# Optimization experiments

Hardware: AMD Instinct MI355X
Metric: run time of the kernel (lower is better)

## Reference

```python
import jax, jax.numpy as jnp
import numpy as np

N_NODES = 50000
N_EDGES = 800000
HEADS = 4
IN_CH = 64
# hidden_dims=[32,64] reversed -> per-head out channels [64, 32]; concat=True
C1, C2 = 64, 32          # layer per-head channels
OUT_CH = 64              # conv_recon per-head channels, concat=False
NEG_SLOPE = 0.2


def gat_conv(x, edge_src, edge_dst, W, a_src, a_dst, b, concat):
    """PyG GATConv (v1) forward, eval mode (no dropout).
    x: [N, F_in]; W: [F_in, H*C]; a_src/a_dst: [H, C]; b: [H*C] or [C].
    edge (j -> i): messages flow edge_src -> edge_dst; softmax grouped by dst.
    """
    N = x.shape[0]
    H, C = a_src.shape
    h = (x @ W).reshape(N, H, C)                    # [N, H, C]
    al_s = jnp.einsum('nhc,hc->nh', h, a_src)       # [N, H]
    al_d = jnp.einsum('nhc,hc->nh', h, a_dst)       # [N, H]
    e = al_s[edge_src] + al_d[edge_dst]             # [E, H]
    e = jax.nn.leaky_relu(e, negative_slope=NEG_SLOPE)
    # segment softmax over incoming edges of each dst node
    m = jax.ops.segment_max(e, edge_dst, num_segments=N)          # [N, H]
    ex = jnp.exp(e - m[edge_dst])                                  # [E, H]
    s = jax.ops.segment_sum(ex, edge_dst, num_segments=N)         # [N, H]
    alpha = ex / (s[edge_dst] + 1e-16)                             # [E, H]
    msg = h[edge_src] * alpha[:, :, None]                          # [E, H, C]
    out = jax.ops.segment_sum(msg, edge_dst, num_segments=N)      # [N, H, C]
    out = out.reshape(N, H * C) if concat else out.mean(axis=1)
    return out + b


def setup_inputs() -> dict:
    key = jax.random.key(0)
    ks = jax.random.split(key, 16)
    sc = 0.1
    inp = {
        'x': jax.random.normal(ks[0], (N_NODES, IN_CH), jnp.float32),
        'edge_index': jax.random.randint(ks[1], (2, N_EDGES), 0, N_NODES, jnp.int64),
        # layer 1: in 64 -> 4 heads x 64, concat -> 256
        'W1': jax.random.normal(ks[2], (IN_CH, HEADS * C1), jnp.float32) * sc,
        'a1_src': jax.random.normal(ks[3], (HEADS, C1), jnp.float32) * sc,
        'a1_dst': jax.random.normal(ks[4], (HEADS, C1), jnp.float32) * sc,
        'b1': jnp.zeros((HEADS * C1,), jnp.float32),
        # layer 2: in 256 -> 4 heads x 32, concat -> 128
        'W2': jax.random.normal(ks[5], (HEADS * C1, HEADS * C2), jnp.float32) * sc,
        'a2_src': jax.random.normal(ks[6], (HEADS, C2), jnp.float32) * sc,
        'a2_dst': jax.random.normal(ks[7], (HEADS, C2), jnp.float32) * sc,
        'b2': jnp.zeros((HEADS * C2,), jnp.float32),
        # conv_recon: in 128 -> 4 heads x 64, concat=False (mean) -> 64
        'W3': jax.random.normal(ks[8], (HEADS * C2, HEADS * OUT_CH), jnp.float32) * sc,
        'a3_src': jax.random.normal(ks[9], (HEADS, OUT_CH), jnp.float32) * sc,
        'a3_dst': jax.random.normal(ks[10], (HEADS, OUT_CH), jnp.float32) * sc,
        'b3': jnp.zeros((OUT_CH,), jnp.float32),
    }
    return inp


def reference(x, edge_index, W1, a1_src, a1_dst, b1, W2, a2_src, a2_dst, b2,
              W3, a3_src, a3_dst, b3):
    src, dst = edge_index[0], edge_index[1]
    # used_DSBN=False -> no norm/ReLU between layers (matches torch forward)
    h = gat_conv(x, src, dst, W1, a1_src, a1_dst, b1, concat=True)
    h = gat_conv(h, src, dst, W2, a2_src, a2_dst, b2, concat=True)
    recon = gat_conv(h, src, dst, W3, a3_src, a3_dst, b3, concat=False)
    return recon
```

## Files before the change

### kernel.cpp

```cpp
#include <hip/hip_runtime.h>
#include <hip/hip_bf16.h>

#define HEADS 4

typedef __attribute__((ext_vector_type(4))) float f32x4;
typedef __attribute__((ext_vector_type(8))) short s16x8;

__device__ __forceinline__ float u2f(unsigned short u) {
    return __uint_as_float(((unsigned)u) << 16);
}
__device__ __forceinline__ unsigned short rne(float v) {
    unsigned b = __float_as_uint(v);
    return (unsigned short)((b + 0x7FFF + ((b >> 16) & 1)) >> 16);
}
__device__ __forceinline__ float ld1(const float* p) { return *p; }
__device__ __forceinline__ float ld1(const __hip_bfloat16* p) {
    return u2f(*reinterpret_cast<const unsigned short*>(p));
}
__device__ __forceinline__ float2 ld2(const float* p) { return *reinterpret_cast<const float2*>(p); }
__device__ __forceinline__ float2 ld2(const __hip_bfloat16* p) {
    ushort2 u = *reinterpret_cast<const ushort2*>(p);
    return make_float2(u2f(u.x), u2f(u.y));
}
__device__ __forceinline__ float4 ld4(const float* p) { return *reinterpret_cast<const float4*>(p); }
__device__ __forceinline__ float4 ld4(const __hip_bfloat16* p) {
    ushort4 u = *reinterpret_cast<const ushort4*>(p);
    return make_float4(u2f(u.x), u2f(u.y), u2f(u.z), u2f(u.w));
}
__device__ __forceinline__ void st1(float* p, float v) { *p = v; }
__device__ __forceinline__ void st1(__hip_bfloat16* p, float v) {
    *reinterpret_cast<unsigned short*>(p) = rne(v);
}
__device__ __forceinline__ void st2(float* p, float a, float b) {
    *reinterpret_cast<float2*>(p) = make_float2(a, b);
}
__device__ __forceinline__ void st2(__hip_bfloat16* p, float a, float b) {
    *reinterpret_cast<ushort2*>(p) = make_ushort2(rne(a), rne(b));
}
__device__ __forceinline__ void st4(float* p, float4 v) { *reinterpret_cast<float4*>(p) = v; }
__device__ __forceinline__ void st4(__hip_bfloat16* p, float4 v) {
    *reinterpret_cast<ushort4*>(p) = make_ushort4(rne(v.x), rne(v.y), rne(v.z), rne(v.w));
}

__device__ __forceinline__ int detect64(const int* __restrict__ e) {
    return ((e[1] | e[3] | e[5] | e[7]) == 0) ? 1 : 0;
}
__device__ __forceinline__ int edge_elem(const int* e, size_t idx, int is64) {
    return is64 ? e[2 * idx] : e[idx];
}

__global__ void deg_kernel(const int* __restrict__ eidx, int* __restrict__ deg, int E, int N) {
    int e = blockIdx.x * blockDim.x + threadIdx.x;
    if (e < E) {
        int is64 = detect64(eidx);
        int d = edge_elem(eidx, (size_t)E + e, is64);
        if ((unsigned)d < (unsigned)N) atomicAdd(&deg[d], 1);
    }
}

__global__ void reduce_kernel(const int* __restrict__ deg, int* __restrict__ bsum, int n) {
    __shared__ int sdata[256];
    int base = blockIdx.x * 1024;
    int t = threadIdx.x;
    int v = 0;
#pragma unroll
    for (int j = 0; j < 4; ++j) {
        int i = base + t + j * 256;
        if (i < n) v += deg[i];
    }
    sdata[t] = v;
    __syncthreads();
    for (int off = 128; off > 0; off >>= 1) {
        if (t < off) sdata[t] += sdata[t + off];
        __syncthreads();
    }
    if (t == 0) bsum[blockIdx.x] = sdata[0];
}

__global__ void scan_bsum_kernel(const int* __restrict__ bsum, int* __restrict__ boff,
                                 int nb, int* __restrict__ totalp) {
    int lane = threadIdx.x;
    int carry = 0;
    for (int base = 0; base < nb; base += 64) {
        int i = base + lane;
        int v = (i < nb) ? bsum[i] : 0;
        int inc = v;
        for (int off = 1; off < 64; off <<= 1) {
            int tt = __shfl_up(inc, off);
            if (lane >= off) inc += tt;
        }
        if (i < nb) boff[i] = carry + inc - v;
        carry += __shfl(inc, 63);
    }
    if (lane == 0) *totalp = carry;
}

__global__ void block_scan_kernel(const int* __restrict__ deg, const int* __restrict__ boff,
                                  int* __restrict__ rowptr, int* __restrict__ cursor, int n) {
    __shared__ int wsum[4];
    int base = blockIdx.x * 1024;
    int t = threadIdx.x;
    int lane = t & 63, w = t >> 6;
    int v[4];
    int lsum = 0;
#pragma unroll
    for (int j = 0; j < 4; ++j) {
        int i = base + t * 4 + j;
        v[j] = (i < n) ? deg[i] : 0;
        lsum += v[j];
    }
    int inc = lsum;
    for (int off = 1; off < 64; off <<= 1) {
        int tt = __shfl_up(inc, off);
        if (lane >= off) inc += tt;
    }
    if (lane == 63) wsum[w] = inc;
    __syncthreads();
    int woff = 0;
    for (int i = 0; i < w; ++i) woff += wsum[i];
    int ex = boff[blockIdx.x] + woff + inc - lsum;
#pragma unroll
    for (int j = 0; j < 4; ++j) {
        int i = base + t * 4 + j;
        if (i < n) { rowptr[i] = ex; cursor[i] = ex; }
        ex += v[j];
    }
}

__global__ void scatter_kernel(const int* __restrict__ eidx, int* __restrict__ cursor,
                               int* __restrict__ csr_src, int E, int N) {
    int e = blockIdx.x * blockDim.x + threadIdx.x;
    if (e < E) {
        int is64 = detect64(eidx);
        int s = edge_elem(eidx, (size_t)e, is64);
        int d = edge_elem(eidx, (size_t)E + e, is64);
        if ((unsigned)d < (unsigned)N && (unsigned)s < (unsigned)N) {
            int pos = atomicAdd(&cursor[d], 1);
            csr_src[pos] = s;
        }
    }
}

__global__ void prep_kernel(const float* __restrict__ x,
                            const float* __restrict__ W1, const float* __restrict__ W2,
                            const float* __restrict__ W3, const float* __restrict__ b1,
                            const float* __restrict__ a1s, const float* __restrict__ a1d,
                            const float* __restrict__ a3s, const float* __restrict__ a3d,
                            __hip_bfloat16* __restrict__ xb,
                            __hip_bfloat16* __restrict__ Bt3, __hip_bfloat16* __restrict__ BtF,
                            float* __restrict__ bias12,
                            float* __restrict__ ps1, float* __restrict__ pd1,
                            float* __restrict__ ps3, float* __restrict__ pd3, int n8) {
    int b = blockIdx.x, t = threadIdx.x;
    int nXB = (n8 + 255) / 256;
    if (b < nXB) {
        int i = b * 256 + t;
        if (i < n8) {
            float4 a = *reinterpret_cast<const float4*>(&x[(size_t)i * 8]);
            float4 c = *reinterpret_cast<const float4*>(&x[(size_t)i * 8 + 4]);
            st4(&xb[(size_t)i * 8], a);
            st4(&xb[(size_t)i * 8 + 4], c);
        }
        return;
    }
    b -= nXB;
    if (b < 128) {
        int idx = b * 256 + t;
        int c = idx >> 9, r = idx & 511;
        int h = r >> 7, kk = r & 127;
        st1(&Bt3[idx], W3[(size_t)kk * 256 + h * 64 + c] * 0.25f);
        return;
    }
    b -= 128;
    if (b < 128) {
        int idx = b * 256 + t;
        int m = idx >> 8, k = idx & 255;
        int h = k >> 6, kin = k & 63;
        float acc = 0.f;
        for (int c = 0; c < 64; ++c)
            acc += W1[(size_t)kin * 256 + h * 64 + c] * W2[(size_t)(h * 64 + c) * 128 + m];
        st1(&BtF[idx], acc);
        return;
    }
    b -= 128;
    if (b < 1) {
        if (t < 128) {
            float acc = 0.f;
            for (int j = 0; j < 256; ++j) acc += b1[j] * W2[(size_t)j * 128 + t];
            bias12[t] = acc;
        }
        return;
    }
    b -= 1;
    if (b < 1) {
        int h = t >> 6, k = t & 63;
        float ss = 0.f, sd = 0.f;
        for (int c = 0; c < 64; ++c) {
            float w = W1[(size_t)k * 256 + h * 64 + c];
            ss += w * a1s[h * 64 + c];
            sd += w * a1d[h * 64 + c];
        }
        ps1[t] = ss;
        pd1[t] = sd;
        return;
    }
    b -= 1;
    if (b < 2) {
        int idx = b * 256 + t;
        int h = idx >> 7, k = idx & 127;
        float ss = 0.f, sd = 0.f;
        for (int c = 0; c < 64; ++c) {
            float w = W3[(size_t)k * 256 + h * 64 + c];
            ss += w * a3s[h * 64 + c];
            sd += w * a3d[h * 64 + c];
        }
        ps3[idx] = ss;
        pd3[idx] = sd;
        return;
    }
}

template <int K, typename T>
__global__ void alx_kernel(const T* __restrict__ x, const float* __restrict__ ps,
                           const float* __restrict__ pd, float* __restrict__ als,
                           float* __restrict__ ald, int N) {
    int idx = blockIdx.x * blockDim.x + threadIdx.x;
    if (idx >= N * 4) return;
    int n = idx >> 2, h = idx & 3;
    const T* row = x + (size_t)n * K;
    const float* vs = ps + h * K;
    const float* vd = pd + h * K;
    float ss = 0.f, sd = 0.f;
#pragma unroll
    for (int c = 0; c < K; c += 4) {
        float4 v = ld4(&row[c]);
        float4 a = *reinterpret_cast<const float4*>(&vs[c]);
        float4 b = *reinterpret_cast<const float4*>(&vd[c]);
        ss += v.x * a.x + v.y * a.y + v.z * a.z + v.w * a.w;
        sd += v.x * b.x + v.y * b.y + v.z * b.z + v.w * b.w;
    }
    als[idx] = ss;
    ald[idx] = sd;
}

template <int C, typename T>
__global__ void al_kernel(const T* __restrict__ h,
                          const float* __restrict__ a_src, const float* __restrict__ a_dst,
                          float* __restrict__ al_s, float* __restrict__ al_d, int N) {
    int idx = blockIdx.x * blockDim.x + threadIdx.x;
    if (idx >= N * HEADS) return;
    int n = idx >> 2, hd = idx & 3;
    const T* row = h + (size_t)n * HEADS * C + hd * C;
    float ss = 0.f, sd = 0.f;
#pragma unroll
    for (int c = 0; c < C; c += 4) {
        float4 v = ld4(&row[c]);
        float4 as = *reinterpret_cast<const float4*>(&a_src[hd * C + c]);
        float4 ad = *reinterpret_cast<const float4*>(&a_dst[hd * C + c]);
        ss += v.x * as.x + v.y * as.y + v.z * as.z + v.w * as.w;
        sd += v.x * ad.x + v.y * ad.y + v.z * ad.z + v.w * ad.w;
    }
    al_s[idx] = ss;
    al_d[idx] = sd;
}

template <int K, typename TIN, typename TOUT>
__global__ void gather_pre_kernel(const TIN* __restrict__ x, const float* __restrict__ als,
                                  const float* __restrict__ ald, const int* __restrict__ rowptr,
                                  const int* __restrict__ csr, TOUT* __restrict__ agg, int N) {
    constexpr int V = K / 64;
    int wave = (blockIdx.x * blockDim.x + threadIdx.x) >> 6;
    int lane = threadIdx.x & 63;
    if (wave >= N) return;
    int h4 = lane & 3, e4 = lane >> 2;
    float aldv = ald[wave * 4 + h4];
    float s0 = 0.f, s1 = 0.f, s2 = 0.f, s3 = 0.f;
    float acc[4][V] = {};
    int beg = rowptr[wave], end = rowptr[wave + 1];
    for (int kc = beg; kc < end; kc += 16) {
        int cnt = end - kc;
        if (cnt > 16) cnt = 16;
        int j = kc + e4;
        int src = csr[(j < end) ? j : beg];
        float e = als[src * 4 + h4] + aldv;
        e = fmaxf(e, 0.2f * e);
        float myw = __expf(e);
        if (cnt == 16) {
            int sj[16];
#pragma unroll
            for (int jj = 0; jj < 16; ++jj) sj[jj] = __shfl(src, jj * 4);
            if (V == 1) {
                float pv[16];
#pragma unroll
                for (int jj = 0; jj < 16; ++jj) pv[jj] = ld1(&x[(size_t)sj[jj] * K + lane]);
#pragma unroll
                for (int jj = 0; jj < 16; ++jj) {
                    float w0 = __shfl(myw, jj * 4 + 0), w1 = __shfl(myw, jj * 4 + 1);
                    float w2 = __shfl(myw, jj * 4 + 2), w3 = __shfl(myw, jj * 4 + 3);
                    s0 += w0; s1 += w1; s2 += w2; s3 += w3;
                    acc[0][0] += w0 * pv[jj]; acc[1][0] += w1 * pv[jj];
                    acc[2][0] += w2 * pv[jj]; acc[3][0] += w3 * pv[jj];
                }
            } else {
                float2 pv[16];
#pragma unroll
                for (int jj = 0; jj < 16; ++jj) pv[jj] = ld2(&x[(size_t)sj[jj] * K + lane * 2]);
#pragma unroll
                for (int jj = 0; jj < 16; ++jj) {
                    float w0 = __shfl(myw, jj * 4 + 0), w1 = __shfl(myw, jj * 4 + 1);
                    float w2 = __shfl(myw, jj * 4 + 2), w3 = __shfl(myw, jj * 4 + 3);
                    s0 += w0; s1 += w1; s2 += w2; s3 += w3;
                    acc[0][0] += w0 * pv[jj].x; acc[0][1] += w0 * pv[jj].y;
                    acc[1][0] += w1 * pv[jj].x; acc[1][1] += w1 * pv[jj].y;
                    acc[2][0] += w2 * pv[jj].x; acc[2][1] += w2 * pv[jj].y;
                    acc[3][0] += w3 * pv[jj].x; acc[3][1] += w3 * pv[jj].y;
                }
            }
        } else {
            for (int jj = 0; jj < cnt; ++jj) {
                int sjj = __shfl(src, jj * 4);
                float w0 = __shfl(myw, jj * 4 + 0), w1 = __shfl(myw, jj * 4 + 1);
                float w2 = __shfl(myw, jj * 4 + 2), w3 = __shfl(myw, jj * 4 + 3);
                s0 += w0; s1 += w1; s2 += w2; s3 += w3;
                if (V == 1) {
                    float v = ld1(&x[(size_t)sjj * K + lane]);
                    acc[0][0] += w0 * v; acc[1][0] += w1 * v;
                    acc[2][0] += w2 * v; acc[3][0] += w3 * v;
                } else {
                    float2 v = ld2(&x[(size_t)sjj * K + lane * 2]);
                    acc[0][0] += w0 * v.x; acc[0][1] += w0 * v.y;
                    acc[1][0] += w1 * v.x; acc[1][1] += w1 * v.y;
                    acc[2][0] += w2 * v.x; acc[2][1] += w2 * v.y;
                    acc[3][0] += w3 * v.x; acc[3][1] += w3 * v.y;
                }
            }
        }
    }
    float inv[4] = {1.f / (s0 + 1e-16f), 1.f / (s1 + 1e-16f),
                    1.f / (s2 + 1e-16f), 1.f / (s3 + 1e-16f)};
    size_t o = (size_t)wave * 4 * K;
#pragma unroll
    for (int h = 0; h < 4; ++h) {
        if (V == 1) {
            st1(&agg[o + h * K + lane], acc[h][0] * inv[h]);
        } else {
            st2(&agg[o + h * K + lane * 2], acc[h][0] * inv[h], acc[h][1] * inv[h]);
        }
    }
}

template <typename TIN, typename TOUT>
__global__ void gather_post32_alx_kernel(const TIN* __restrict__ h2, const float* __restrict__ als,
                                         const float* __restrict__ ald, const int* __restrict__ rowptr,
                                         const int* __restrict__ csr, const float* __restrict__ bias,
                                         const float* __restrict__ ps3, const float* __restrict__ pd3,
                                         TOUT* __restrict__ outp,
                                         float* __restrict__ als3, float* __restrict__ ald3, int N) {
    int wave = (blockIdx.x * blockDim.x + threadIdx.x) >> 6;
    int lane = threadIdx.x & 63;
    if (wave >= N) return;
    int h4 = lane & 3, e4 = lane >> 2;
    int hh = lane >> 4, l16 = lane & 15;
    float aldv = ald[wave * 4 + h4];
    float s = 0.f, a0 = 0.f, a1 = 0.f;
    int beg = rowptr[wave], end = rowptr[wave + 1];
    for (int kc = beg; kc < end; kc += 16) {
        int cnt = end - kc;
        if (cnt > 16) cnt = 16;
        int j = kc + e4;
        int src = csr[(j < end) ? j : beg];
        float e = als[src * 4 + h4] + aldv;
        e = fmaxf(e, 0.2f * e);
        float myw = __expf(e);
        if (cnt == 16) {
            int sj[16];
#pragma unroll
            for (int jj = 0; jj < 16; ++jj) sj[jj] = __shfl(src, jj * 4);
            float2 pv[16];
#pragma unroll
            for (int jj = 0; jj < 16; ++jj)
                pv[jj] = ld2(&h2[(size_t)sj[jj] * 128 + hh * 32 + l16 * 2]);
#pragma unroll
            for (int jj = 0; jj < 16; ++jj) {
                float w = __shfl(myw, jj * 4 + hh);
                s += w;
                a0 += w * pv[jj].x;
                a1 += w * pv[jj].y;
            }
        } else {
            for (int jj = 0; jj < cnt; ++jj) {
                int sjj = __shfl(src, jj * 4);
                float w = __shfl(myw, jj * 4 + hh);
                s += w;
                float2 v = ld2(&h2[(size_t)sjj * 128 + hh * 32 + l16 * 2]);
                a0 += w * v.x;
                a1 += w * v.y;
            }
        }
    }
    float inv = 1.f / (s + 1e-16f);
    int c = hh * 32 + l16 * 2;
    float v0 = a0 * inv + bias[c];
    float v1 = a1 * inv + bias[c + 1];
    st2(&outp[(size_t)wave * 128 + c], v0, v1);

    float sArr[4], dArr[4];
#pragma unroll
    for (int h = 0; h < 4; ++h) {
        float2 vs = *reinterpret_cast<const float2*>(&ps3[h * 128 + c]);
        float2 vd = *reinterpret_cast<const float2*>(&pd3[h * 128 + c]);
        sArr[h] = v0 * vs.x + v1 * vs.y;
        dArr[h] = v0 * vd.x + v1 * vd.y;
    }
#pragma unroll
    for (int off = 1; off < 64; off <<= 1) {
#pragma unroll
        for (int h = 0; h < 4; ++h) {
            sArr[h] += __shfl_xor(sArr[h], off);
            dArr[h] += __shfl_xor(dArr[h], off);
        }
    }
    if (lane < 4) {
        float os = (lane == 0) ? sArr[0] : (lane == 1) ? sArr[1] : (lane == 2) ? sArr[2] : sArr[3];
        float od = (lane == 0) ? dArr[0] : (lane == 1) ? dArr[1] : (lane == 2) ? dArr[2] : dArr[3];
        als3[wave * 4 + lane] = os;
        ald3[wave * 4 + lane] = od;
    }
}

template <typename TOUT>
__global__ __launch_bounds__(256) void mfma_gemm_kernel(
    const __hip_bfloat16* __restrict__ A, int lda, int aSel,
    const __hip_bfloat16* __restrict__ Bt,
    TOUT* __restrict__ O, int ldo,
    const float* __restrict__ bias, int N, int K) {
    __shared__ __hip_bfloat16 As[128][40];
    __shared__ __hip_bfloat16 Bs[64][40];
    int col0 = blockIdx.x * 64;
    int row0 = blockIdx.y * 128;
    int aOff = aSel ? col0 : 0;
    int tid = threadIdx.x;
    int wv = tid >> 6, lane = tid & 63;
    int g = lane >> 4, l16 = lane & 15;
    f32x4 acc[2][4] = {};

    for (int k0 = 0; k0 < K; k0 += 32) {
#pragma unroll
        for (int i = 0; i < 2; ++i) {
            int idx = tid + i * 256;
            int r = idx >> 2, h4 = idx & 3;
            int gr = row0 + r;
            uint4 v = make_uint4(0, 0, 0, 0);
            if (gr < N) v = *reinterpret_cast<const uint4*>(&A[(size_t)gr * lda + aOff + k0 + h4 * 8]);
            *reinterpret_cast<uint4*>(&As[r][h4 * 8]) = v;
        }
        {
            int r = tid >> 2, h4 = tid & 3;
            uint4 v = *reinterpret_cast<const uint4*>(&Bt[(size_t)(col0 + r) * K + k0 + h4 * 8]);
            *reinterpret_cast<uint4*>(&Bs[r][h4 * 8]) = v;
        }
        __syncthreads();
        s16x8 af[2], bf[4];
#pragma unroll
        for (int m = 0; m < 2; ++m)
            af[m] = *reinterpret_cast<const s16x8*>(&As[wv * 32 + m * 16 + l16][g * 8]);
#pragma unroll
        for (int n = 0; n < 4; ++n)
            bf[n] = *reinterpret_cast<const s16x8*>(&Bs[n * 16 + l16][g * 8]);
#pragma unroll
        for (int m = 0; m < 2; ++m)
#pragma unroll
            for (int n = 0; n < 4; ++n)
                acc[m][n] = __builtin_amdgcn_mfma_f32_16x16x32_bf16(af[m], bf[n], acc[m][n], 0, 0, 0);
        __syncthreads();
    }
#pragma unroll
    for (int m = 0; m < 2; ++m) {
#pragma unroll
        for (int rr = 0; rr < 4; ++rr) {
            int row = row0 + wv * 32 + m * 16 + g * 4 + rr;
            if (row < N) {
#pragma unroll
                for (int n = 0; n < 4; ++n) {
                    int col = col0 + n * 16 + l16;
                    float v = acc[m][n][rr];
                    if (bias) v += bias[col];
                    st1(&O[(size_t)row * ldo + col], v);
                }
            }
        }
    }
}

extern "C" void kernel_launch(void* const* d_in, const int* in_sizes, int n_in,
                              void* d_out, int out_size, void* d_ws, size_t ws_size,
                              hipStream_t stream) {
    const float* x      = (const float*)d_in[0];
    const int*   eidx   = (const int*)d_in[1];
    const float* W1     = (const float*)d_in[2];
    const float* a1_src = (const float*)d_in[3];
    const float* a1_dst = (const float*)d_in[4];
    const float* b1     = (const float*)d_in[5];
    const float* W2     = (const float*)d_in[6];
    const float* a2_src = (const float*)d_in[7];
    const float* a2_dst = (const float*)d_in[8];
    const float* b2     = (const float*)d_in[9];
    const float* W3     = (const float*)d_in[10];
    const float* a3_src = (const float*)d_in[11];
    const float* a3_dst = (const float*)d_in[12];
    const float* b3     = (const float*)d_in[13];
    float* out = (float*)d_out;

    const int N = in_sizes[0] / 64;
    const int E = in_sizes[1] / 2;
    const int NB = (N + 1023) / 1024;

    int* rowptr = (int*)d_ws;
    int* deg    = rowptr + (N + 1);
    int* cursor = deg + N;
    int* csr    = cursor + N;
    int* bsum   = csr + E;
    int* boff   = bsum + NB;
    uintptr_t pa = (uintptr_t)(boff + NB);
    pa = (pa + 255) & ~(uintptr_t)255;
    float* als  = (float*)pa;
    float* ald  = als + (size_t)N * 4;
    float* als3 = ald + (size_t)N * 4;
    float* ald3 = als3 + (size_t)N * 4;
    float* ps1  = ald3 + (size_t)N * 4;
    float* pd1  = ps1 + 256;
    float* ps3  = pd1 + 256;
    float* pd3  = ps3 + 512;
    float* bias12 = pd3 + 512;
    __hip_bfloat16* Bt3 = (__hip_bfloat16*)(bias12 + 128);
    __hip_bfloat16* BtF = Bt3 + 64 * 512;
    uintptr_t pf = (uintptr_t)(BtF + 128 * 256);
    pf = (pf + 255) & ~(uintptr_t)255;
    float* F    = (float*)pf;

    __hip_bfloat16* xb    = (__hip_bfloat16*)F;
    __hip_bfloat16* agg1b = (__hip_bfloat16*)(F + (size_t)N * 32);
    __hip_bfloat16* h2b   = (__hip_bfloat16*)(F + (size_t)N * 160);
    __hip_bfloat16* out2b = (__hip_bfloat16*)(F + (size_t)N * 224);
    __hip_bfloat16* agg3  = (__hip_bfloat16*)(F + (size_t)N * 288);

    hipMemsetAsync(deg, 0, (size_t)N * sizeof(int), stream);
    deg_kernel<<<(E + 255) / 256, 256, 0, stream>>>(eidx, deg, E, N);
    reduce_kernel<<<NB, 256, 0, stream>>>(deg, bsum, N);
    scan_bsum_kernel<<<1, 64, 0, stream>>>(bsum, boff, NB, rowptr + N);
    block_scan_kernel<<<NB, 256, 0, stream>>>(deg, boff, rowptr, cursor, N);
    scatter_kernel<<<(E + 255) / 256, 256, 0, stream>>>(eidx, cursor, csr, E, N);

    const int n8 = N * 8;
    const int nXB = (n8 + 255) / 256;
    prep_kernel<<<nXB + 128 + 128 + 1 + 1 + 2, 256, 0, stream>>>(
        x, W1, W2, W3, b1, a1_src, a1_dst, a3_src, a3_dst,
        xb, Bt3, BtF, bias12, ps1, pd1, ps3, pd3, n8);

    const int alBlocks  = (N * HEADS + 255) / 256;
    const int aggBlocks = (N + 3) / 4;
    const int rowB128   = (N + 127) / 128;

    alx_kernel<64, float><<<alBlocks, 256, 0, stream>>>(x, ps1, pd1, als, ald, N);
    gather_pre_kernel<64, __hip_bfloat16, __hip_bfloat16><<<aggBlocks, 256, 0, stream>>>(
        xb, als, ald, rowptr, csr, agg1b, N);
    mfma_gemm_kernel<__hip_bfloat16><<<dim3(2, rowB128), 256, 0, stream>>>(
        agg1b, 256, 0, BtF, h2b, 128, bias12, N, 256);

    al_kernel<32, __hip_bfloat16><<<alBlocks, 256, 0, stream>>>(h2b, a2_src, a2_dst, als, ald, N);
    gather_post32_alx_kernel<__hip_bfloat16, __hip_bfloat16><<<aggBlocks, 256, 0, stream>>>(
        h2b, als, ald, rowptr, csr, b2, ps3, pd3, out2b, als3, ald3, N);

    gather_pre_kernel<128, __hip_bfloat16, __hip_bfloat16><<<aggBlocks, 256, 0, stream>>>(
        out2b, als3, ald3, rowptr, csr, agg3, N);
    mfma_gemm_kernel<float><<<dim3(1, rowB128), 256, 0, stream>>>(
        agg3, 512, 0, Bt3, out, 64, b3, N, 512);
}
```

Baseline: 353.8 us.

## Fuse x bf16 conversion with layer-1 attention logits; stage edge weights in LDS

The x-to-bf16 conversion moves out of the prep kernel and merges with the layer-1 attention-logit computation into one kernel. It reduces partial dot products across 8 lanes with xor shuffles, so x is read once instead of twice. In the gather kernels, per-edge softmax weights go into a per-wave LDS buffer read as float4, and source indices come straight from csr instead of through cross-lane shuffles. There is no barrier between the LDS write and the reads; this relies on wave-synchronous execution, and a later chunk's write could race with earlier reads.

```diff
diff --git a/kernel.cpp b/kernel.cpp
--- a/kernel.cpp
+++ b/kernel.cpp
@@ -141,29 +141,15 @@
     }
 }
 
-__global__ void prep_kernel(const float* __restrict__ x,
-                            const float* __restrict__ W1, const float* __restrict__ W2,
-                            const float* __restrict__ W3, const float* __restrict__ b1,
-                            const float* __restrict__ a1s, const float* __restrict__ a1d,
-                            const float* __restrict__ a3s, const float* __restrict__ a3d,
-                            __hip_bfloat16* __restrict__ xb,
-                            __hip_bfloat16* __restrict__ Bt3, __hip_bfloat16* __restrict__ BtF,
-                            float* __restrict__ bias12,
-                            float* __restrict__ ps1, float* __restrict__ pd1,
-                            float* __restrict__ ps3, float* __restrict__ pd3, int n8) {
+__global__ void prep0_kernel(const float* __restrict__ W1, const float* __restrict__ W2,
+                             const float* __restrict__ W3, const float* __restrict__ b1,
+                             const float* __restrict__ a1s, const float* __restrict__ a1d,
+                             const float* __restrict__ a3s, const float* __restrict__ a3d,
+                             __hip_bfloat16* __restrict__ Bt3, __hip_bfloat16* __restrict__ BtF,
+                             float* __restrict__ bias12,
+                             float* __restrict__ ps1, float* __restrict__ pd1,
+                             float* __restrict__ ps3, float* __restrict__ pd3) {
     int b = blockIdx.x, t = threadIdx.x;
-    int nXB = (n8 + 255) / 256;
-    if (b < nXB) {
-        int i = b * 256 + t;
-        if (i < n8) {
-            float4 a = *reinterpret_cast<const float4*>(&x[(size_t)i * 8]);
-            float4 c = *reinterpret_cast<const float4*>(&x[(size_t)i * 8 + 4]);
-            st4(&xb[(size_t)i * 8], a);
-            st4(&xb[(size_t)i * 8 + 4], c);
-        }
-        return;
-    }
-    b -= nXB;
     if (b < 128) {
         int idx = b * 256 + t;
         int c = idx >> 9, r = idx & 511;
@@ -220,27 +206,41 @@
     }
 }
 
-template <int K, typename T>
-__global__ void alx_kernel(const T* __restrict__ x, const float* __restrict__ ps,
-                           const float* __restrict__ pd, float* __restrict__ als,
-                           float* __restrict__ ald, int N) {
-    int idx = blockIdx.x * blockDim.x + threadIdx.x;
-    if (idx >= N * 4) return;
-    int n = idx >> 2, h = idx & 3;
-    const T* row = x + (size_t)n * K;
-    const float* vs = ps + h * K;
-    const float* vd = pd + h * K;
-    float ss = 0.f, sd = 0.f;
-#pragma unroll
-    for (int c = 0; c < K; c += 4) {
-        float4 v = ld4(&row[c]);
-        float4 a = *reinterpret_cast<const float4*>(&vs[c]);
-        float4 b = *reinterpret_cast<const float4*>(&vd[c]);
-        ss += v.x * a.x + v.y * a.y + v.z * a.z + v.w * a.w;
-        sd += v.x * b.x + v.y * b.y + v.z * b.z + v.w * b.w;
-    }
-    als[idx] = ss;
-    ald[idx] = sd;
+__global__ void xconv_alx_kernel(const float* __restrict__ x, const float* __restrict__ ps1,
+                                 const float* __restrict__ pd1, __hip_bfloat16* __restrict__ xb,
+                                 float* __restrict__ als, float* __restrict__ ald, int n8) {
+    int i = blockIdx.x * blockDim.x + threadIdx.x;
+    if (i >= n8) return;
+    int r = i >> 3, sub = i & 7;
+    int cbase = sub * 8;
+    float4 a = *reinterpret_cast<const float4*>(&x[(size_t)i * 8]);
+    float4 c = *reinterpret_cast<const float4*>(&x[(size_t)i * 8 + 4]);
+    st4(&xb[(size_t)i * 8], a);
+    st4(&xb[(size_t)i * 8 + 4], c);
+    float ss[4], sd[4];
+#pragma unroll
+    for (int h = 0; h < 4; ++h) {
+        float4 s0 = *reinterpret_cast<const float4*>(&ps1[h * 64 + cbase]);
+        float4 s1 = *reinterpret_cast<const float4*>(&ps1[h * 64 + cbase + 4]);
+        float4 d0 = *reinterpret_cast<const float4*>(&pd1[h * 64 + cbase]);
+        float4 d1 = *reinterpret_cast<const float4*>(&pd1[h * 64 + cbase + 4]);
+        ss[h] = a.x * s0.x + a.y * s0.y + a.z * s0.z + a.w * s0.w
+              + c.x * s1.x + c.y * s1.y + c.z * s1.z + c.w * s1.w;
+        sd[h] = a.x * d0.x + a.y * d0.y + a.z * d0.z + a.w * d0.w
+              + c.x * d1.x + c.y * d1.y + c.z * d1.z + c.w * d1.w;
+    }
+#pragma unroll
+    for (int off = 1; off < 8; off <<= 1) {
+#pragma unroll
+        for (int h = 0; h < 4; ++h) {
+            ss[h] += __shfl_xor(ss[h], off);
+            sd[h] += __shfl_xor(sd[h], off);
+        }
+    }
+    if (sub == 0) {
+        *reinterpret_cast<float4*>(&als[(size_t)r * 4]) = make_float4(ss[0], ss[1], ss[2], ss[3]);
+        *reinterpret_cast<float4*>(&ald[(size_t)r * 4]) = make_float4(sd[0], sd[1], sd[2], sd[3]);
+    }
 }
 
 template <int C, typename T>
@@ -265,10 +265,13 @@
 }
 
 template <int K, typename TIN, typename TOUT>
-__global__ void gather_pre_kernel(const TIN* __restrict__ x, const float* __restrict__ als,
-                                  const float* __restrict__ ald, const int* __restrict__ rowptr,
-                                  const int* __restrict__ csr, TOUT* __restrict__ agg, int N) {
+__global__ __launch_bounds__(256) void gather_pre_kernel(
+    const TIN* __restrict__ x, const float* __restrict__ als,
+    const float* __restrict__ ald, const int* __restrict__ rowptr,
+    const int* __restrict__ csr, TOUT* __restrict__ agg, int N) {
     constexpr int V = K / 64;
+    __shared__ float wlds[4][64];
+    int wv = threadIdx.x >> 6;
     int wave = (blockIdx.x * blockDim.x + threadIdx.x) >> 6;
     int lane = threadIdx.x & 63;
     if (wave >= N) return;
@@ -284,22 +287,21 @@
         int src = csr[(j < end) ? j : beg];
         float e = als[src * 4 + h4] + aldv;
         e = fmaxf(e, 0.2f * e);
-        float myw = __expf(e);
+        wlds[wv][lane] = __expf(e);
         if (cnt == 16) {
             int sj[16];
 #pragma unroll
-            for (int jj = 0; jj < 16; ++jj) sj[jj] = __shfl(src, jj * 4);
+            for (int jj = 0; jj < 16; ++jj) sj[jj] = csr[kc + jj];
             if (V == 1) {
                 float pv[16];
 #pragma unroll
                 for (int jj = 0; jj < 16; ++jj) pv[jj] = ld1(&x[(size_t)sj[jj] * K + lane]);
 #pragma unroll
                 for (int jj = 0; jj < 16; ++jj) {
-                    float w0 = __shfl(myw, jj * 4 + 0), w1 = __shfl(myw, jj * 4 + 1);
-                    float w2 = __shfl(myw, jj * 4 + 2), w3 = __shfl(myw, jj * 4 + 3);
-                    s0 += w0; s1 += w1; s2 += w2; s3 += w3;
-                    acc[0][0] += w0 * pv[jj]; acc[1][0] += w1 * pv[jj];
-                    acc[2][0] += w2 * pv[jj]; acc[3][0] += w3 * pv[jj];
+                    float4 w = *reinterpret_cast<const float4*>(&wlds[wv][jj * 4]);
+                    s0 += w.x; s1 += w.y; s2 += w.z; s3 += w.w;
+                    acc[0][0] += w.x * pv[jj]; acc[1][0] += w.y * pv[jj];
+                    acc[2][0] += w.z * pv[jj]; acc[3][0] += w.w * pv[jj];
                 }
             } else {
                 float2 pv[16];
@@ -307,31 +309,29 @@
                 for (int jj = 0; jj < 16; ++jj) pv[jj] = ld2(&x[(size_t)sj[jj] * K + lane * 2]);
 #pragma unroll
                 for (int jj = 0; jj < 16; ++jj) {
-                    float w0 = __shfl(myw, jj * 4 + 0), w1 = __shfl(myw, jj * 4 + 1);
-                    float w2 = __shfl(myw, jj * 4 + 2), w3 = __shfl(myw, jj * 4 + 3);
-                    s0 += w0; s1 += w1; s2 += w2; s3 += w3;
-                    acc[0][0] += w0 * pv[jj].x; acc[0][1] += w0 * pv[jj].y;
-                    acc[1][0] += w1 * pv[jj].x; acc[1][1] += w1 * pv[jj].y;
-                    acc[2][0] += w2 * pv[jj].x; acc[2][1] += w2 * pv[jj].y;
-                    acc[3][0] += w3 * pv[jj].x; acc[3][1] += w3 * pv[jj].y;
+                    float4 w = *reinterpret_cast<const float4*>(&wlds[wv][jj * 4]);
+                    s0 += w.x; s1 += w.y; s2 += w.z; s3 += w.w;
+                    acc[0][0] += w.x * pv[jj].x; acc[0][1] += w.x * pv[jj].y;
+                    acc[1][0] += w.y * pv[jj].x; acc[1][1] += w.y * pv[jj].y;
+                    acc[2][0] += w.z * pv[jj].x; acc[2][1] += w.z * pv[jj].y;
+                    acc[3][0] += w.w * pv[jj].x; acc[3][1] += w.w * pv[jj].y;
                 }
             }
         } else {
             for (int jj = 0; jj < cnt; ++jj) {
-                int sjj = __shfl(src, jj * 4);
-                float w0 = __shfl(myw, jj * 4 + 0), w1 = __shfl(myw, jj * 4 + 1);
-                float w2 = __shfl(myw, jj * 4 + 2), w3 = __shfl(myw, jj * 4 + 3);
-                s0 += w0; s1 += w1; s2 += w2; s3 += w3;
+                int sjj = csr[kc + jj];
+                float4 w = *reinterpret_cast<const float4*>(&wlds[wv][jj * 4]);
+                s0 += w.x; s1 += w.y; s2 += w.z; s3 += w.w;
                 if (V == 1) {
                     float v = ld1(&x[(size_t)sjj * K + lane]);
-                    acc[0][0] += w0 * v; acc[1][0] += w1 * v;
-                    acc[2][0] += w2 * v; acc[3][0] += w3 * v;
+                    acc[0][0] += w.x * v; acc[1][0] += w.y * v;
+                    acc[2][0] += w.z * v; acc[3][0] += w.w * v;
                 } else {
                     float2 v = ld2(&x[(size_t)sjj * K + lane * 2]);
-                    acc[0][0] += w0 * v.x; acc[0][1] += w0 * v.y;
-                    acc[1][0] += w1 * v.x; acc[1][1] += w1 * v.y;
-                    acc[2][0] += w2 * v.x; acc[2][1] += w2 * v.y;
-                    acc[3][0] += w3 * v.x; acc[3][1] += w3 * v.y;
+                    acc[0][0] += w.x * v.x; acc[0][1] += w.x * v.y;
+                    acc[1][0] += w.y * v.x; acc[1][1] += w.y * v.y;
+                    acc[2][0] += w.z * v.x; acc[2][1] += w.z * v.y;
+                    acc[3][0] += w.w * v.x; acc[3][1] += w.w * v.y;
                 }
             }
         }
@@ -350,12 +350,15 @@
 }
 
 template <typename TIN, typename TOUT>
-__global__ void gather_post32_alx_kernel(const TIN* __restrict__ h2, const float* __restrict__ als,
-                                         const float* __restrict__ ald, const int* __restrict__ rowptr,
-                                         const int* __restrict__ csr, const float* __restrict__ bias,
-                                         const float* __restrict__ ps3, const float* __restrict__ pd3,
-                                         TOUT* __restrict__ outp,
-                                         float* __restrict__ als3, float* __restrict__ ald3, int N) {
+__global__ __launch_bounds__(256) void gather_post32_alx_kernel(
+    const TIN* __restrict__ h2, const float* __restrict__ als,
+    const float* __restrict__ ald, const int* __restrict__ rowptr,
+    const int* __restrict__ csr, const float* __restrict__ bias,
+    const float* __restrict__ ps3, const float* __restrict__ pd3,
+    TOUT* __restrict__ outp,
+    float* __restrict__ als3, float* __restrict__ ald3, int N) {
+    __shared__ float wlds[4][64];
+    int wv = threadIdx.x >> 6;
     int wave = (blockIdx.x * blockDim.x + threadIdx.x) >> 6;
     int lane = threadIdx.x & 63;
     if (wave >= N) return;
@@ -371,26 +374,26 @@
         int src = csr[(j < end) ? j : beg];
         float e = als[src * 4 + h4] + aldv;
         e = fmaxf(e, 0.2f * e);
-        float myw = __expf(e);
+        wlds[wv][lane] = __expf(e);
         if (cnt == 16) {
             int sj[16];
 #pragma unroll
-            for (int jj = 0; jj < 16; ++jj) sj[jj] = __shfl(src, jj * 4);
+            for (int jj = 0; jj < 16; ++jj) sj[jj] = csr[kc + jj];
             float2 pv[16];
 #pragma unroll
             for (int jj = 0; jj < 16; ++jj)
                 pv[jj] = ld2(&h2[(size_t)sj[jj] * 128 + hh * 32 + l16 * 2]);
 #pragma unroll
             for (int jj = 0; jj < 16; ++jj) {
-                float w = __shfl(myw, jj * 4 + hh);
+                float w = wlds[wv][jj * 4 + hh];
                 s += w;
                 a0 += w * pv[jj].x;
                 a1 += w * pv[jj].y;
             }
         } else {
             for (int jj = 0; jj < cnt; ++jj) {
-                int sjj = __shfl(src, jj * 4);
-                float w = __shfl(myw, jj * 4 + hh);
+                int sjj = csr[kc + jj];
+                float w = wlds[wv][jj * 4 + hh];
                 s += w;
                 float2 v = ld2(&h2[(size_t)sjj * 128 + hh * 32 + l16 * 2]);
                 a0 += w * v.x;
@@ -551,17 +554,16 @@
     block_scan_kernel<<<NB, 256, 0, stream>>>(deg, boff, rowptr, cursor, N);
     scatter_kernel<<<(E + 255) / 256, 256, 0, stream>>>(eidx, cursor, csr, E, N);
 
+    prep0_kernel<<<128 + 128 + 1 + 1 + 2, 256, 0, stream>>>(
+        W1, W2, W3, b1, a1_src, a1_dst, a3_src, a3_dst,
+        Bt3, BtF, bias12, ps1, pd1, ps3, pd3);
     const int n8 = N * 8;
-    const int nXB = (n8 + 255) / 256;
-    prep_kernel<<<nXB + 128 + 128 + 1 + 1 + 2, 256, 0, stream>>>(
-        x, W1, W2, W3, b1, a1_src, a1_dst, a3_src, a3_dst,
-        xb, Bt3, BtF, bias12, ps1, pd1, ps3, pd3, n8);
+    xconv_alx_kernel<<<(n8 + 255) / 256, 256, 0, stream>>>(x, ps1, pd1, xb, als, ald, n8);
 
     const int alBlocks  = (N * HEADS + 255) / 256;
     const int aggBlocks = (N + 3) / 4;
     const int rowB128   = (N + 127) / 128;
 
-    alx_kernel<64, float><<<alBlocks, 256, 0, stream>>>(x, ps1, pd1, als, ald, N);
     gather_pre_kernel<64, __hip_bfloat16, __hip_bfloat16><<<aggBlocks, 256, 0, stream>>>(
         xb, als, ald, rowptr, csr, agg1b, N);
     mfma_gemm_kernel<__hip_bfloat16><<<dim3(2, rowB128), 256, 0, stream>>>(
```

Measured after the change: 361.1 us. 2.1% more time.
